# Kernel optimization log

Hardware: AMD Instinct MI355X
Metric: run time of the kernel (lower is better)

Reference implementation:

```python
import jax, jax.numpy as jnp
import numpy as np

N_GROUPS = 16  # images per batch; rois[:,0] holds group id, equal-sized groups of 16
HID = 512
EPS = 1e-5


def conv2d(x, w):
    # 3x3 conv, padding=1, no bias; NCHW / OIHW
    return jax.lax.conv_general_dilated(
        x, w, window_strides=(1, 1), padding=[(1, 1), (1, 1)],
        dimension_numbers=("NCHW", "OIHW", "NCHW"))


def group_norm1(x, gamma, beta):
    # nn.GroupNorm(1, C, affine=True): normalize over (C,H,W) per sample
    mu = jnp.mean(x, axis=(1, 2, 3), keepdims=True)
    var = jnp.var(x, axis=(1, 2, 3), keepdims=True)
    xn = (x - mu) * jax.lax.rsqrt(var + EPS)
    return xn * gamma[None, :, None, None] + beta[None, :, None, None]


def setup_inputs() -> dict:
    key = jax.random.key(0)
    ks = jax.random.split(key, 16)
    N, n = 256, 256 // N_GROUPS
    C_in, C, S, H, W = 2304, HID, 5, 7, 7
    status = jax.random.normal(ks[0], (N, 2), jnp.float32)
    gid = jnp.repeat(jnp.arange(N_GROUPS, dtype=jnp.float32), n)[:, None]
    boxes = jax.random.uniform(ks[1], (N, 4), jnp.float32)
    rois = jnp.concatenate([gid, boxes], axis=1)  # [N,5]
    bbox_feat = jax.random.normal(ks[2], (N, C_in, 1, H, W), jnp.float32)
    w = lambda k, shape: jax.random.normal(k, shape, jnp.float32) * 0.02
    return {
        "status": status, "rois": rois, "bbox_feat": bbox_feat,
        "w_reduce": w(ks[3], (C, C_in, 3, 3)),
        "w_q1": w(ks[4], (C, S, 3, 3)), "w_q2": w(ks[5], (C, S, 3, 3)),
        "w_k1": w(ks[6], (C, C, 3, 3)), "w_v1": w(ks[7], (C, C, 3, 3)),
        "w_k2": w(ks[8], (C, C, 3, 3)), "w_v2": w(ks[9], (C, C, 3, 3)),
        "w_c1": w(ks[10], (C, C, 3, 3)), "w_c2": w(ks[11], (C, C, 3, 3)),
        "gamma": jnp.ones((C,), jnp.float32),
        "beta": jnp.zeros((C,), jnp.float32),
    }


def reference(status, rois, bbox_feat, w_reduce, w_q1, w_q2, w_k1, w_v1,
              w_k2, w_v2, w_c1, w_c2, gamma, beta):
    N = bbox_feat.shape[0]
    H, W = bbox_feat.shape[-2], bbox_feat.shape[-1]
    n = N // N_GROUPS
    scale = 1.0 / np.sqrt(HID)

    feat = conv2d(bbox_feat[:, :, 0], w_reduce)  # [N, C, H, W]

    boxes = rois[:, 1:]  # [N, 4]
    s1 = jnp.concatenate([status[:, 0:1], boxes], axis=1)  # [N, 5]
    s2 = jnp.concatenate([status[:, 1:2], boxes], axis=1)
    s1 = jnp.broadcast_to(s1[:, :, None, None], (N, 5, H, W))
    s2 = jnp.broadcast_to(s2[:, :, None, None], (N, 5, H, W))

    q1, q2 = conv2d(s1, w_q1), conv2d(s2, w_q2)
    k1, v1 = conv2d(feat, w_k1), conv2d(feat, w_v1)
    k2, v2 = conv2d(feat, w_k2), conv2d(feat, w_v2)

    grp = lambda t: t.reshape(N_GROUPS, n, *t.shape[1:])  # [G, n, C, H, W]

    def branch(q, k, v, w_out):
        # per-group attention: att[i,j,h,w] = <q_i, k_j>_C / sqrt(C)
        att = jnp.einsum("gichw,gjchw->gijhw", grp(q), grp(k)) * scale
        att = jax.nn.softmax(att, axis=2)  # softmax over key index j
        virt = jnp.einsum("gijhw,gjchw->gichw", att, grp(v))
        virt = virt.reshape(N, HID, H, W)
        h = jax.nn.relu(group_norm1(virt, gamma, beta))
        h = conv2d(h, w_out)  # dropout is identity in eval mode
        return (feat + h)[:, :, None]  # [N, C, 1, H, W]

    out1 = branch(q1, k1, v1, w_c1)
    out2 = branch(q2, k2, v2, w_c2)
    return (out1, out2)
```

## Files before the change

### kernel.cpp

```cpp
#include <hip/hip_runtime.h>
#include <stdint.h>

typedef unsigned short u16;
typedef short short8 __attribute__((ext_vector_type(8)));
typedef float f32x4 __attribute__((ext_vector_type(4)));

#define NS 256
#define CIN 2304
#define CH 512
#define HW 49
#define MTOT (NS*HW)

__device__ __forceinline__ float b2f(u16 u){
    union { unsigned int v; float f; } x; x.v = ((unsigned int)u) << 16; return x.f;
}
__device__ __forceinline__ u16 f2b(float f){
    unsigned int u = __builtin_bit_cast(unsigned int, f);
    u += 0x7FFFu + ((u >> 16) & 1u);
    return (u16)(u >> 16);
}
__device__ __forceinline__ u16 load_as_bf16(const void* p, size_t i, int isf32){
    return isf32 ? f2b(((const float*)p)[i]) : ((const u16*)p)[i];
}

__device__ __forceinline__ void gload16(const u16* g, u16* l){
    __builtin_amdgcn_global_load_lds((const __attribute__((address_space(1))) void*)g,
                                     (__attribute__((address_space(3))) void*)l,
                                     16, 0, 0);
}

__global__ void k_detect(const u16* __restrict__ src, int* __restrict__ flag){
    int cnt = 0;
    for (int i = threadIdx.x; i < 8192; i += 256){
        int e = (src[i] >> 7) & 0xFF;
        cnt += (e >= 0x90);
    }
    for (int off = 32; off; off >>= 1) cnt += __shfl_down(cnt, off, 64);
    __shared__ int sh[4];
    int wave = threadIdx.x >> 6, lane = threadIdx.x & 63;
    if (lane == 0) sh[wave] = cnt;
    __syncthreads();
    if (threadIdx.x == 0)
        flag[0] = (sh[0] + sh[1] + sh[2] + sh[3] > 200) ? 1 : 0;
}

__global__ void k_zero(u16* __restrict__ p, int n){
    int i = blockIdx.x*256 + threadIdx.x;
    if (i < n) p[i] = 0;
}

__global__ void k_convert_small(const void* __restrict__ src, u16* __restrict__ dst,
                                int n, const int* __restrict__ flag){
    const int isf32 = flag[0];
    for (int i = blockIdx.x*256 + threadIdx.x; i < n; i += gridDim.x*256)
        dst[i] = load_as_bf16(src, i, isf32);
}

__global__ void k_transpose_in(const void* __restrict__ src, u16* __restrict__ dst,
                               const int* __restrict__ flag){
    const int isf32 = flag[0];
    __shared__ u16 tile[64*50];
    const int n = blockIdx.x;
    const int c0 = blockIdx.y * 64;
    const size_t sbase = ((size_t)n*CIN + c0)*HW;
    for (int idx = threadIdx.x; idx < 64*49; idx += 256){
        int cc = idx / 49, hw = idx - cc*49;
        tile[cc*50 + hw] = load_as_bf16(src, sbase + cc*HW + hw, isf32);
    }
    __syncthreads();
    u16* d = dst + (size_t)n*HW*CIN + c0;
    for (int idx = threadIdx.x; idx < 49*64; idx += 256){
        int hw = idx >> 6, cc = idx & 63;
        d[(size_t)hw*CIN + cc] = tile[cc*50 + hw];
    }
}

__global__ void k_transpose_w(const void* __restrict__ w, u16* __restrict__ wt,
                              int Cin, const int* __restrict__ flag){
    const int isf32 = flag[0];
    size_t total = (size_t)CH * Cin * 9;
    for (size_t d = (size_t)blockIdx.x*blockDim.x + threadIdx.x; d < total;
         d += (size_t)gridDim.x*blockDim.x){
        int c  = (int)(d % Cin);
        size_t t = d / Cin;
        int kk = (int)(t % 9);
        int co = (int)(t / 9);
        wt[d] = load_as_bf16(w, ((size_t)co*Cin + c)*9 + kk, isf32);
    }
}

__global__ __launch_bounds__(256, 2) void k_conv3x3(
        const u16* __restrict__ in_t, const u16* __restrict__ w_t, int Cin,
        const u16* __restrict__ zpage,
        u16* __restrict__ out_cl,
        const u16* __restrict__ feat_res, void* __restrict__ out_base,
        int mode, int branch, const int* __restrict__ dtf)
{
    __shared__ __align__(16) u16 As0[128*64];
    __shared__ __align__(16) u16 Bs0[128*64];
    __shared__ __align__(16) u16 As1[128*64];
    __shared__ __align__(16) u16 Bs1[128*64];
    const int tid  = threadIdx.x;
    const int wave = tid >> 6, lane = tid & 63;
    const int m0  = blockIdx.x * 128;
    const int co0 = blockIdx.y * 128;

    const int lr  = tid >> 3;
    const int sl  = tid & 7;
    const int swz = (sl ^ (lr & 7)) * 8;

    int nA[4], yA[4], xA[4];
#pragma unroll
    for (int s = 0; s < 4; ++s){
        int m = m0 + lr + 32*s;
        nA[s] = m / 49;
        int hw = m - nA[s]*49;
        yA[s] = hw / 7; xA[s] = hw - yA[s]*7;
    }

    const u16* aPtr[4];
    const u16* bPtr[4];
#pragma unroll
    for (int s = 0; s < 4; ++s)
        bPtr[s] = w_t + (size_t)(co0 + lr + 32*s)*9*Cin + swz;
    int kkS = 0, c0S = 0;

    auto recompTaps = [&](){
        int dy = kkS/3 - 1, dx = kkS - (kkS/3)*3 - 1;
#pragma unroll
        for (int s = 0; s < 4; ++s){
            int yy = yA[s] + dy, xx = xA[s] + dx;
            bool valid = (yy >= 0) & (yy < 7) & (xx >= 0) & (xx < 7);
            aPtr[s] = valid ? in_t + (size_t)(nA[s]*49 + yy*7 + xx)*Cin + swz
                            : zpage + swz;
        }
    };
    recompTaps();

    int dstOff[4];
#pragma unroll
    for (int s = 0; s < 4; ++s) dstOff[s] = (wave*8 + s*32)*64;

    auto STAGE = [&](u16* A, u16* B){
#pragma unroll
        for (int s = 0; s < 4; ++s){
            gload16(aPtr[s], A + dstOff[s]);
            gload16(bPtr[s], B + dstOff[s]);
        }
    };
    auto ADV = [&](){
#pragma unroll
        for (int s = 0; s < 4; ++s){ aPtr[s] += 64; bPtr[s] += 64; }
        c0S += 64;
        if (c0S == Cin){
            c0S = 0; ++kkS;
            if (kkS < 9) recompTaps();
        }
    };

    f32x4 acc[4][4];
#pragma unroll
    for (int i = 0; i < 4; ++i)
#pragma unroll
        for (int j = 0; j < 4; ++j)
            acc[i][j] = (f32x4){0.f, 0.f, 0.f, 0.f};

    const int wm = (wave & 1) * 64, wn = (wave >> 1) * 64;
    const int rA0 = wm + (lane & 15);
    const int rB0 = wn + (lane & 15);
    const int sl0 = (((lane >> 4)    ) ^ (lane & 7)) * 8;
    const int sl1 = ((4 + (lane >> 4)) ^ (lane & 7)) * 8;

    auto COMPUTE = [&](const u16* A, const u16* B){
        short8 af[4], bf[4];
#pragma unroll
        for (int i = 0; i < 4; ++i) af[i] = *(const short8*)&A[(rA0 + i*16)*64 + sl0];
#pragma unroll
        for (int j = 0; j < 4; ++j) bf[j] = *(const short8*)&B[(rB0 + j*16)*64 + sl0];
#pragma unroll
        for (int i = 0; i < 4; ++i)
#pragma unroll
            for (int j = 0; j < 4; ++j)
                acc[i][j] = __builtin_amdgcn_mfma_f32_16x16x32_bf16(
                                af[i], bf[j], acc[i][j], 0, 0, 0);
#pragma unroll
        for (int i = 0; i < 4; ++i) af[i] = *(const short8*)&A[(rA0 + i*16)*64 + sl1];
#pragma unroll
        for (int j = 0; j < 4; ++j) bf[j] = *(const short8*)&B[(rB0 + j*16)*64 + sl1];
#pragma unroll
        for (int i = 0; i < 4; ++i)
#pragma unroll
            for (int j = 0; j < 4; ++j)
                acc[i][j] = __builtin_amdgcn_mfma_f32_16x16x32_bf16(
                                af[i], bf[j], acc[i][j], 0, 0, 0);
    };

    const int NK = 9 * (Cin >> 6);
    STAGE(As0, Bs0); ADV();
    __syncthreads();
    for (int t = 0; t < NK; t += 2){
        STAGE(As1, Bs1); ADV();
        COMPUTE(As0, Bs0);
        __syncthreads();
        if (t + 2 < NK){ STAGE(As0, Bs0); ADV(); }
        COMPUTE(As1, Bs1);
        __syncthreads();
    }

    const int isf32 = (mode == 1) ? dtf[0] : 0;
#pragma unroll
    for (int i = 0; i < 4; ++i){
        int mbase = m0 + wm + i*16 + (lane >> 4)*4;
#pragma unroll
        for (int j = 0; j < 4; ++j){
            int co = co0 + wn + j*16 + (lane & 15);
#pragma unroll
            for (int r = 0; r < 4; ++r){
                int m = mbase + r;
                float v = acc[i][j][r];
                if (mode == 0){
                    out_cl[(size_t)(co >> 9)*((size_t)MTOT*CH)
                           + (size_t)m*CH + (co & 511)] = f2b(v);
                } else {
                    float res = b2f(feat_res[(size_t)m*CH + co]);
                    int n = m / 49, hw = m - (m/49)*49;
                    size_t off = (size_t)branch*MTOT*CH + ((size_t)n*CH + co)*HW + hw;
                    float o = v + res;
                    if (isf32) ((float*)out_base)[off] = o;
                    else       ((u16*)out_base)[off]   = f2b(o);
                }
            }
        }
    }
}

__global__ void k_qconv(const u16* __restrict__ status, const u16* __restrict__ rois,
                        const u16* __restrict__ wq, u16* __restrict__ q_t, int branch){
    const int hw = blockIdx.x;
    const int n0 = blockIdx.y * 64;
    const int co = threadIdx.x;
    const int y = hw / 7, x = hw - (hw/7)*7;

    __shared__ float sv[64][5];
    for (int idx = threadIdx.x; idx < 64*5; idx += 512){
        int n = idx / 5, c = idx - n*5;
        sv[n][c] = (c == 0) ? b2f(status[(n0 + n)*2 + branch])
                            : b2f(rois[(n0 + n)*5 + c]);
    }
    __syncthreads();

    float wsum[5];
#pragma unroll
    for (int c = 0; c < 5; ++c){
        float s = 0.f;
#pragma unroll
        for (int ky = 0; ky < 3; ++ky){
            int yy = y + ky - 1; if (yy < 0 || yy >= 7) continue;
#pragma unroll
            for (int kx = 0; kx < 3; ++kx){
                int xx = x + kx - 1; if (xx < 0 || xx >= 7) continue;
                s += b2f(wq[(co*5 + c)*9 + ky*3 + kx]);
            }
        }
        wsum[c] = s;
    }

    u16* dst = q_t + ((size_t)n0*HW + hw)*CH + co;
    for (int n = 0; n < 64; ++n){
        float acc = sv[n][0]*wsum[0] + sv[n][1]*wsum[1] + sv[n][2]*wsum[2]
                  + sv[n][3]*wsum[3] + sv[n][4]*wsum[4];
        dst[(size_t)n*HW*CH] = f2b(acc);
    }
}

__global__ void k_att(const u16* __restrict__ q_t, const u16* __restrict__ k_t,
                      const u16* __restrict__ v_t, u16* __restrict__ virt_t){
    __shared__ u16 qs[16*520], ks[16*520], vs[16*520];
    __shared__ float ls[256], ps[256];
    const int hw = blockIdx.x, g = blockIdx.y;
    const int tid = threadIdx.x;
    for (int idx = tid; idx < 16*512; idx += 256){
        int i = idx >> 9, c = idx & 511;
        size_t m = (size_t)(g*16 + i)*HW + hw;
        qs[i*520 + c] = q_t[m*CH + c];
        ks[i*520 + c] = k_t[m*CH + c];
        vs[i*520 + c] = v_t[m*CH + c];
    }
    __syncthreads();
    const int i = tid >> 4, j = tid & 15;
    float dot = 0.f;
    for (int c = 0; c < 512; ++c) dot += b2f(qs[i*520 + c]) * b2f(ks[j*520 + c]);
    ls[tid] = dot * 0.04419417382415922f;
    __syncthreads();
    float mx = -1e30f;
    for (int jj = 0; jj < 16; ++jj) mx = fmaxf(mx, ls[i*16 + jj]);
    float ssum = 0.f;
    for (int jj = 0; jj < 16; ++jj) ssum += __expf(ls[i*16 + jj] - mx);
    ps[tid] = __expf(ls[tid] - mx) / ssum;
    __syncthreads();
    const int c0 = tid & 15, ii = tid >> 4;
    for (int c = c0; c < 512; c += 16){
        float a = 0.f;
        for (int jj = 0; jj < 16; ++jj) a += ps[ii*16 + jj] * b2f(vs[jj*520 + c]);
        virt_t[((size_t)(g*16 + ii)*HW + hw)*CH + c] = f2b(a);
    }
}

__global__ void k_stats(const u16* __restrict__ virt_t, float* __restrict__ stats){
    const int n = blockIdx.x;
    const u16* p = virt_t + (size_t)n * (CH*HW);
    float s = 0.f, s2 = 0.f;
    for (int idx = threadIdx.x; idx < CH*HW; idx += 256){
        float v = b2f(p[idx]); s += v; s2 += v*v;
    }
    for (int off = 32; off; off >>= 1){
        s  += __shfl_down(s,  off, 64);
        s2 += __shfl_down(s2, off, 64);
    }
    __shared__ float bs[4], bs2[4];
    int wave = threadIdx.x >> 6, lane = threadIdx.x & 63;
    if (lane == 0){ bs[wave] = s; bs2[wave] = s2; }
    __syncthreads();
    if (threadIdx.x == 0){
        float t = 0.f, t2 = 0.f;
        for (int w = 0; w < 4; ++w){ t += bs[w]; t2 += bs2[w]; }
        float mean = t / (float)(CH*HW);
        float var  = t2 / (float)(CH*HW) - mean*mean;
        stats[n*2]   = mean;
        stats[n*2+1] = rsqrtf(var + 1e-5f);
    }
}

__global__ void k_norm(const u16* __restrict__ virt_t, const float* __restrict__ stats,
                       const u16* __restrict__ gamma, const u16* __restrict__ beta,
                       u16* __restrict__ h_t){
    size_t idx = (size_t)blockIdx.x*256 + threadIdx.x;
    if (idx >= (size_t)NS*HW*CH) return;
    int c = (int)(idx & 511);
    int m = (int)(idx >> 9);
    int n = m / 49;
    float v = b2f(virt_t[idx]);
    float h = (v - stats[n*2]) * stats[n*2+1] * b2f(gamma[c]) + b2f(beta[c]);
    h_t[idx] = f2b(fmaxf(h, 0.f));
}

extern "C" void kernel_launch(void* const* d_in, const int* in_sizes, int n_in,
                              void* d_out, int out_size, void* d_ws, size_t ws_size,
                              hipStream_t stream) {
    const void* status   = d_in[0];
    const void* rois     = d_in[1];
    const void* bbox     = d_in[2];
    const void* w_reduce = d_in[3];
    const void* w_q1     = d_in[4];
    const void* w_q2     = d_in[5];
    const void* w_k1     = d_in[6];
    const void* w_v1     = d_in[7];
    const void* w_k2     = d_in[8];
    const void* w_v2     = d_in[9];
    const void* w_c1     = d_in[10];
    const void* w_c2     = d_in[11];
    const void* gamma    = d_in[12];
    const void* beta     = d_in[13];

    char* p = (char*)d_ws;
    const size_t SZ_INT  = (size_t)MTOT*CIN*2;
    const size_t SZ_WRT  = (size_t)CH*9*CIN*2;
    const size_t SZ_T    = (size_t)MTOT*CH*2;
    const size_t SZ_WT   = (size_t)CH*9*CH*2;

    u16* in_t  = (u16*)p;
    u16* w_r_t = (u16*)(p + SZ_INT);
    char* p2   = p + SZ_INT + SZ_WRT;
    u16* wt[6];
    for (int i = 0; i < 6; ++i) wt[i] = (u16*)(p2 + i*SZ_WT);
    u16* feat_t = (u16*)(p2 + 6*SZ_WT);
    char* p3 = p2 + 6*SZ_WT + SZ_T;
    float* stats    = (float*)p3;
    int*   flag     = (int*)(p3 + 4096);
    u16*   status_c = (u16*)(p3 + 8192);
    u16*   rois_c   = status_c + 1024;
    u16*   gamma_c  = rois_c + 2048;
    u16*   beta_c   = gamma_c + 512;
    u16*   wq_c0    = beta_c + 512;
    u16*   wq_c1    = wq_c0 + CH*5*9;
    u16*   zp       = wq_c1 + CH*5*9;
    u16* q_t    = (u16*)p;
    u16* k_t    = (u16*)(p + SZ_T);
    u16* v_t    = (u16*)(p + 2*SZ_T);
    u16* virt_t = (u16*)(p + 3*SZ_T);
    u16* h_t    = w_r_t;

    k_detect<<<1, 256, 0, stream>>>((const u16*)bbox, flag);
    k_zero<<<16, 256, 0, stream>>>(zp, 4096);
    k_transpose_in<<<dim3(NS, CIN/64), 256, 0, stream>>>(bbox, in_t, flag);
    k_transpose_w<<<1024, 256, 0, stream>>>(w_reduce, w_r_t, CIN, flag);
    const void* wsrc[6] = {w_k1, w_v1, w_k2, w_v2, w_c1, w_c2};
    for (int i = 0; i < 6; ++i)
        k_transpose_w<<<512, 256, 0, stream>>>(wsrc[i], wt[i], CH, flag);
    k_convert_small<<<2, 256, 0, stream>>>(status, status_c, NS*2, flag);
    k_convert_small<<<5, 256, 0, stream>>>(rois, rois_c, NS*5, flag);
    k_convert_small<<<2, 256, 0, stream>>>(gamma, gamma_c, CH, flag);
    k_convert_small<<<2, 256, 0, stream>>>(beta, beta_c, CH, flag);
    k_convert_small<<<90, 256, 0, stream>>>(w_q1, wq_c0, CH*5*9, flag);
    k_convert_small<<<90, 256, 0, stream>>>(w_q2, wq_c1, CH*5*9, flag);

    k_conv3x3<<<dim3(MTOT/128, CH/128), 256, 0, stream>>>(
        in_t, w_r_t, CIN, zp, feat_t, nullptr, nullptr, 0, 0, flag);

    for (int br = 0; br < 2; ++br){
        k_qconv<<<dim3(HW, 4), 512, 0, stream>>>(status_c, rois_c,
                                                 br ? wq_c1 : wq_c0, q_t, br);
        k_conv3x3<<<dim3(MTOT/128, 1024/128), 256, 0, stream>>>(
            feat_t, wt[br*2], CH, zp, k_t, nullptr, nullptr, 0, 0, flag);
        k_att<<<dim3(HW, 16), 256, 0, stream>>>(q_t, k_t, v_t, virt_t);
        k_stats<<<NS, 256, 0, stream>>>(virt_t, stats);
        k_norm<<<(NS*HW*CH)/256, 256, 0, stream>>>(virt_t, stats, gamma_c, beta_c, h_t);
        k_conv3x3<<<dim3(MTOT/128, CH/128), 256, 0, stream>>>(
            h_t, wt[4 + br], CH, zp, nullptr, feat_t, d_out, 1, br, flag);
    }
}
```

Measured before the change: 1.340 ms.

## Batch all four K/V convs into one launch, swizzle blocks, stage output via LDS

Merges the per-branch K/V convolutions into a single 2048-output-channel conv launch that writes four contiguous K/V buffers, which removes one launch and gives a larger grid. Workgroup IDs are remapped in strides of eight, apparently to spread neighbouring tiles across XCDs or caches. The residual epilogue now stages results in shared memory so NCHW stores are written coalesced along hw. In exchange the buffers are re-laid out, which needs more scratch memory, and the h_t and weight regions may alias.

```diff
diff --git a/kernel.cpp b/kernel.cpp
--- a/kernel.cpp
+++ b/kernel.cpp
@@ -96,14 +96,23 @@
         const u16* __restrict__ feat_res, void* __restrict__ out_base,
         int mode, int branch, const int* __restrict__ dtf)
 {
-    __shared__ __align__(16) u16 As0[128*64];
-    __shared__ __align__(16) u16 Bs0[128*64];
-    __shared__ __align__(16) u16 As1[128*64];
-    __shared__ __align__(16) u16 Bs1[128*64];
+    __shared__ __align__(16) u16 SH[4*128*64];
+    u16* const As0 = SH;
+    u16* const Bs0 = SH + 128*64;
+    u16* const As1 = SH + 2*128*64;
+    u16* const Bs1 = SH + 3*128*64;
+
     const int tid  = threadIdx.x;
     const int wave = tid >> 6, lane = tid & 63;
-    const int m0  = blockIdx.x * 128;
-    const int co0 = blockIdx.y * 128;
+
+    const int nbx = gridDim.x, nby = gridDim.y;
+    const int nwg = nbx * nby;
+    const int did = blockIdx.x + nbx*blockIdx.y;
+    const int id2 = (did & 7) * (nwg >> 3) + (did >> 3);
+    const int bx  = id2 / nby;
+    const int by  = id2 - bx*nby;
+    const int m0  = bx * 128;
+    const int co0 = by * 128;
 
     const int lr  = tid >> 3;
     const int sl  = tid & 7;
@@ -207,29 +216,48 @@
         __syncthreads();
     }
 
-    const int isf32 = (mode == 1) ? dtf[0] : 0;
-#pragma unroll
-    for (int i = 0; i < 4; ++i){
-        int mbase = m0 + wm + i*16 + (lane >> 4)*4;
-#pragma unroll
-        for (int j = 0; j < 4; ++j){
-            int co = co0 + wn + j*16 + (lane & 15);
-#pragma unroll
-            for (int r = 0; r < 4; ++r){
-                int m = mbase + r;
-                float v = acc[i][j][r];
-                if (mode == 0){
+    if (mode == 0){
+#pragma unroll
+        for (int i = 0; i < 4; ++i){
+            int mbase = m0 + wm + i*16 + (lane >> 4)*4;
+#pragma unroll
+            for (int j = 0; j < 4; ++j){
+                int co = co0 + wn + j*16 + (lane & 15);
+#pragma unroll
+                for (int r = 0; r < 4; ++r){
+                    int m = mbase + r;
                     out_cl[(size_t)(co >> 9)*((size_t)MTOT*CH)
-                           + (size_t)m*CH + (co & 511)] = f2b(v);
-                } else {
-                    float res = b2f(feat_res[(size_t)m*CH + co]);
-                    int n = m / 49, hw = m - (m/49)*49;
-                    size_t off = (size_t)branch*MTOT*CH + ((size_t)n*CH + co)*HW + hw;
-                    float o = v + res;
-                    if (isf32) ((float*)out_base)[off] = o;
-                    else       ((u16*)out_base)[off]   = f2b(o);
+                           + (size_t)m*CH + (co & 511)] = f2b(acc[i][j][r]);
                 }
             }
+        }
+    } else {
+        const int isf32 = dtf[0];
+        float* FO = (float*)SH;
+#pragma unroll
+        for (int i = 0; i < 4; ++i){
+            int mib = wm + i*16 + (lane >> 4)*4;
+#pragma unroll
+            for (int j = 0; j < 4; ++j){
+                int coj = wn + j*16 + (lane & 15);
+#pragma unroll
+                for (int r = 0; r < 4; ++r){
+                    int mi = mib + r;
+                    float res = b2f(feat_res[(size_t)(m0 + mi)*CH + co0 + coj]);
+                    FO[coj*128 + mi] = acc[i][j][r] + res;
+                }
+            }
+        }
+        __syncthreads();
+        for (int idx = tid; idx < 128*128; idx += 256){
+            int coj = idx >> 7, mi = idx & 127;
+            int m = m0 + mi;
+            int n = m / 49, hw = m - n*49;
+            size_t off = (size_t)branch*MTOT*CH
+                       + ((size_t)n*CH + (co0 + coj))*HW + hw;
+            float o = FO[coj*128 + mi];
+            if (isf32) ((float*)out_base)[off] = o;
+            else       ((u16*)out_base)[off]   = f2b(o);
         }
     }
 }
@@ -384,11 +412,10 @@
     u16*   wq_c0    = beta_c + 512;
     u16*   wq_c1    = wq_c0 + CH*5*9;
     u16*   zp       = wq_c1 + CH*5*9;
-    u16* q_t    = (u16*)p;
-    u16* k_t    = (u16*)(p + SZ_T);
-    u16* v_t    = (u16*)(p + 2*SZ_T);
-    u16* virt_t = (u16*)(p + 3*SZ_T);
-    u16* h_t    = w_r_t;
+    u16* kv4    = (u16*)p;
+    u16* q_t    = (u16*)(p + 4*SZ_T);
+    u16* virt_t = (u16*)(p + 5*SZ_T);
+    u16* h_t    = (u16*)p2;
 
     k_detect<<<1, 256, 0, stream>>>((const u16*)bbox, flag);
     k_zero<<<16, 256, 0, stream>>>(zp, 4096);
@@ -407,12 +434,15 @@
     k_conv3x3<<<dim3(MTOT/128, CH/128), 256, 0, stream>>>(
         in_t, w_r_t, CIN, zp, feat_t, nullptr, nullptr, 0, 0, flag);
 
+    k_conv3x3<<<dim3(MTOT/128, 2048/128), 256, 0, stream>>>(
+        feat_t, wt[0], CH, zp, kv4, nullptr, nullptr, 0, 0, flag);
+
     for (int br = 0; br < 2; ++br){
         k_qconv<<<dim3(HW, 4), 512, 0, stream>>>(status_c, rois_c,
                                                  br ? wq_c1 : wq_c0, q_t, br);
-        k_conv3x3<<<dim3(MTOT/128, 1024/128), 256, 0, stream>>>(
-            feat_t, wt[br*2], CH, zp, k_t, nullptr, nullptr, 0, 0, flag);
-        k_att<<<dim3(HW, 16), 256, 0, stream>>>(q_t, k_t, v_t, virt_t);
+        k_att<<<dim3(HW, 16), 256, 0, stream>>>(
+            q_t, kv4 + (size_t)(2*br)*MTOT*CH, kv4 + (size_t)(2*br+1)*MTOT*CH,
+            virt_t);
         k_stats<<<NS, 256, 0, stream>>>(virt_t, stats);
         k_norm<<<(NS*HW*CH)/256, 256, 0, stream>>>(virt_t, stats, gamma_c, beta_c, h_t);
         k_conv3x3<<<dim3(MTOT/128, CH/128), 256, 0, stream>>>(
```

Measured after the change: 1.255 ms. 6.3% less time.
